# Kernel optimization log

Measured on AMD Instinct MI355X. Metric: run time of the kernel, lower is better.

The kernel has to match this reference:

```python
import jax, jax.numpy as jnp
import numpy as np

B, N, C, H = 8, 1024, 768, 12
D = C // H
SCALE = D ** -0.5


def _norm_unbiased(t):
    # per-head-dim standardization with torch's default unbiased std (ddof=1)
    mu = t.mean(axis=-1, keepdims=True)
    var = ((t - mu) ** 2).sum(axis=-1, keepdims=True) / (t.shape[-1] - 1)
    return (t - mu) / jnp.sqrt(var)


def setup_inputs() -> dict:
    key = jax.random.key(0)
    kx, kq, kp, kb = jax.random.split(key, 4)
    x = jax.random.normal(kx, (B, N, C), dtype=jnp.float32)
    # nn.Linear default init ~ U(-1/sqrt(fan_in), 1/sqrt(fan_in)); scale suffices
    s = 1.0 / np.sqrt(C)
    qkv_w = jax.random.uniform(kq, (3 * C, C), minval=-s, maxval=s, dtype=jnp.float32)
    proj_w = jax.random.uniform(kp, (C, C), minval=-s, maxval=s, dtype=jnp.float32)
    proj_b = jax.random.uniform(kb, (C,), minval=-s, maxval=s, dtype=jnp.float32)
    return {"x": x, "qkv_w": qkv_w, "proj_w": proj_w, "proj_b": proj_b}


def reference(x, qkv_w, proj_w, proj_b):
    Bn, Nn, Cn = x.shape
    qkv = x @ qkv_w.T                                   # [B,N,3C]
    qkv = qkv.reshape(Bn, Nn, 3, H, D).transpose(2, 0, 3, 1, 4)  # [3,B,H,N,D]
    q, k, v = qkv[0], qkv[1], qkv[2]
    q = _norm_unbiased(q)
    k = _norm_unbiased(k)
    attn = jax.nn.softmax(jnp.einsum('bhnd,bhmd->bhnm', q, k) * SCALE, axis=-1)
    out = jnp.einsum('bhnm,bhmd->bhnd', attn, v)        # [B,H,N,D]
    out = out.transpose(0, 2, 1, 3).reshape(Bn, Nn, Cn)  # [B,N,C]
    return out @ proj_w.T + proj_b
```

## Files before the change

kernel.cpp:

```cpp
#include <hip/hip_runtime.h>
#include <hip/hip_bf16.h>
#include <stdint.h>

typedef unsigned short u16;
typedef __attribute__((ext_vector_type(8))) short bf16x8;
typedef __attribute__((ext_vector_type(4))) float f32x4;

#define GLDS16(gsrc, ldst) \
  __builtin_amdgcn_global_load_lds((const __attribute__((address_space(1))) uint32_t*)(gsrc), \
                                   (__attribute__((address_space(3))) uint32_t*)(ldst), 16, 0, 0)

__device__ __forceinline__ u16 f2bf(float f) {
  unsigned u = __float_as_uint(f);
  return (u16)((u + 0x7fffu + ((u >> 16) & 1u)) >> 16);
}
__device__ __forceinline__ u16 f2bfr(float f) {
  return (u16)((__float_as_uint(f) + 0x8000u) >> 16);
}
__device__ __forceinline__ float bf2f(u16 v) {
  return __uint_as_float(((unsigned)v) << 16);
}

__global__ void cvt_f2b4(const float* __restrict__ in, u16* __restrict__ out, int n4) {
  int i = blockIdx.x * 256 + threadIdx.x;
  if (i < n4) {
    float4 v = ((const float4*)in)[i];
    ushort4 r;
    r.x = f2bf(v.x); r.y = f2bf(v.y); r.z = f2bf(v.z); r.w = f2bf(v.w);
    ((ushort4*)out)[i] = r;
  }
}

#define GEMM_PREAMBLE(AP, BP)                                              \
  __shared__ __align__(16) u16 As[3][128 * 32];                            \
  __shared__ __align__(16) u16 Bs[3][128 * 32];                            \
  const int tid  = threadIdx.x;                                            \
  const int lane = tid & 63;                                               \
  const int w    = tid >> 6;                                               \
  const int wr   = w >> 1, wc = w & 1;                                     \
  const int m0 = blockIdx.x * 128;                                         \
  const int n0 = blockIdx.y * 128;                                         \
  f32x4 acc[4][4];                                                         \
  for (int m = 0; m < 4; ++m)                                              \
    for (int n = 0; n < 4; ++n) acc[m][n] = (f32x4){0.f, 0.f, 0.f, 0.f};   \
  const int rsel = lane >> 2;                                              \
  const int koff = (((lane & 3) ^ ((lane >> 3) & 3))) * 8;                 \
  const int fr   = lane & 15;                                              \
  const int hi   = lane >> 4;                                              \
  const int slot = (hi ^ ((fr >> 1) & 3)) * 8;                             \
  auto stage = [&](int buf, int kt) {                                      \
    _Pragma("unroll")                                                      \
    for (int t = 0; t < 2; ++t) {                                          \
      const int seg = w * 2 + t;                                           \
      const int rr  = seg * 16 + rsel;                                     \
      GLDS16(AP + (size_t)(m0 + rr) * 768 + kt * 32 + koff,                \
             (char*)As[buf] + seg * 1024);                                 \
      GLDS16(BP + (size_t)(n0 + rr) * 768 + kt * 32 + koff,                \
             (char*)Bs[buf] + seg * 1024);                                 \
    }                                                                      \
  };                                                                       \
  stage(0, 0); stage(1, 1);                                                \
  asm volatile("s_waitcnt vmcnt(4)" ::: "memory");                         \
  __builtin_amdgcn_s_barrier();                                            \
  for (int kt = 0; kt < 24; ++kt) {                                        \
    const int cb = kt % 3;                                                 \
    if (kt + 2 < 24) stage((kt + 2) % 3, kt + 2);                          \
    bf16x8 af[4], bg[4];                                                   \
    _Pragma("unroll")                                                      \
    for (int m = 0; m < 4; ++m)                                            \
      af[m] = *(const bf16x8*)(As[cb] + (wr * 64 + m * 16 + fr) * 32 + slot);\
    _Pragma("unroll")                                                      \
    for (int n = 0; n < 4; ++n)                                            \
      bg[n] = *(const bf16x8*)(Bs[cb] + (wc * 64 + n * 16 + fr) * 32 + slot);\
    _Pragma("unroll")                                                      \
    for (int m = 0; m < 4; ++m)                                            \
      _Pragma("unroll")                                                    \
      for (int n = 0; n < 4; ++n)                                          \
        acc[m][n] = __builtin_amdgcn_mfma_f32_16x16x32_bf16(af[m], bg[n], acc[m][n], 0, 0, 0); \
    if (kt < 23) {                                                         \
      if (kt < 22) asm volatile("s_waitcnt vmcnt(4)" ::: "memory");        \
      else         asm volatile("s_waitcnt vmcnt(0)" ::: "memory");        \
      __builtin_amdgcn_s_barrier();                                        \
    }                                                                      \
  }

__global__ __launch_bounds__(256, 3)
void gemm_qkv(const u16* __restrict__ A, const u16* __restrict__ Bm,
              u16* __restrict__ qb, u16* __restrict__ kb, u16* __restrict__ vt)
{
  GEMM_PREAMBLE(A, Bm)
  const int b     = m0 >> 10;
  const int nrow0 = (m0 & 1023) + wr * 64 + hi * 4;
  const int sec   = n0 / 768;
  const int csb   = (n0 % 768) + wc * 64;
  const int hh    = csb >> 6;
  if (sec < 2) {
    u16* base = (sec == 0 ? qb : kb) + ((size_t)(b * 12 + hh) << 16);
#pragma unroll
    for (int m = 0; m < 4; ++m)
#pragma unroll
      for (int i = 0; i < 4; ++i) {
        float t0 = acc[m][0][i], t1 = acc[m][1][i], t2 = acc[m][2][i], t3 = acc[m][3][i];
        float sum = (t0 + t1) + (t2 + t3);
        sum += __shfl_xor(sum, 1, 64); sum += __shfl_xor(sum, 2, 64);
        sum += __shfl_xor(sum, 4, 64); sum += __shfl_xor(sum, 8, 64);
        const float mu = sum * (1.f / 64.f);
        t0 -= mu; t1 -= mu; t2 -= mu; t3 -= mu;
        float ss = t0 * t0 + t1 * t1 + t2 * t2 + t3 * t3;
        ss += __shfl_xor(ss, 1, 64); ss += __shfl_xor(ss, 2, 64);
        ss += __shfl_xor(ss, 4, 64); ss += __shfl_xor(ss, 8, 64);
        const float scl = rsqrtf(ss * (1.f / 63.f));
        ushort4 pk;
        pk.x = f2bf(t0 * scl); pk.y = f2bf(t1 * scl);
        pk.z = f2bf(t2 * scl); pk.w = f2bf(t3 * scl);
        *(ushort4*)(base + (size_t)(nrow0 + m * 16 + i) * 64 + fr * 4) = pk;
      }
  } else {
    u16* base = vt + ((size_t)(b * 12 + hh) << 16);
#pragma unroll
    for (int nf = 0; nf < 4; ++nf) {
      const int d = nf * 16 + fr;
#pragma unroll
      for (int m = 0; m < 4; ++m) {
        const int vrow = nrow0 + m * 16;
        ushort4 pk;
        pk.x = f2bf(acc[m][nf][0]); pk.y = f2bf(acc[m][nf][1]);
        pk.z = f2bf(acc[m][nf][2]); pk.w = f2bf(acc[m][nf][3]);
        *(ushort4*)(base + (size_t)d * 1024 + vrow) = pk;
      }
    }
  }
}

__global__ __launch_bounds__(256, 3)
void gemm_proj(const u16* __restrict__ A, const u16* __restrict__ Bm,
               const float* __restrict__ bias, float* __restrict__ Cout)
{
  GEMM_PREAMBLE(A, Bm)
  const int r0 = m0 + wr * 64 + hi * 4;
  const int c0 = n0 + wc * 64 + fr;
#pragma unroll
  for (int nf = 0; nf < 4; ++nf) {
    const float bv = bias[c0 + nf * 16];
#pragma unroll
    for (int m = 0; m < 4; ++m)
#pragma unroll
      for (int i = 0; i < 4; ++i)
        Cout[(size_t)(r0 + m * 16 + i) * 768 + c0 + nf * 16] = acc[m][nf][i] + bv;
  }
}

__global__ __launch_bounds__(256, 4)
void attn_fwd(const u16* __restrict__ q, const u16* __restrict__ k,
              const u16* __restrict__ vt, u16* __restrict__ out)
{
  __shared__ __align__(16) u16 Ks[2][64 * 64];
  __shared__ __align__(16) u16 VTs[2][64 * 64];
  __shared__ __align__(16) u16 Ps[4][16 * 64];
  const int tid = threadIdx.x, lane = tid & 63, w = tid >> 6;
  const int bid = (blockIdx.x & 7) * 192 + (blockIdx.x >> 3);
  const int qt = bid & 15;
  const int bh = bid >> 4;
  const int b = bh / 12, h = bh % 12;
  const int fr = lane & 15;
  const int hi = lane >> 4;
  const int fk = hi * 8;

  bf16x8 aq[2];
  {
    const int qrow = qt * 64 + w * 16 + fr;
    const u16* qp = q + ((size_t)bh * 1024 + qrow) * 64;
#pragma unroll
    for (int kk = 0; kk < 2; ++kk)
      aq[kk] = *(const bf16x8*)(qp + kk * 32 + fk);
  }

  bf16x8 ones;
#pragma unroll
  for (int j = 0; j < 8; ++j) ones[j] = (short)0x3F80;

  f32x4 o[4];
  for (int n = 0; n < 4; ++n) o[n] = (f32x4){0.f, 0.f, 0.f, 0.f};
  f32x4 o5 = (f32x4){0.f, 0.f, 0.f, 0.f};

  const int srow = lane >> 3;
  const int sc   = ((lane & 7) ^ srow) * 8;
  const u16* kg = k  + (size_t)bh * 65536;
  const u16* vg = vt + (size_t)bh * 65536;

  auto stage = [&](int buf, int kt) {
#pragma unroll
    for (int t = 0; t < 2; ++t) {
      const int seg = w * 2 + t;
      const int rr = seg * 8 + srow;
      GLDS16(kg + (size_t)(kt * 64 + rr) * 64 + sc,  (char*)Ks[buf]  + seg * 1024);
      GLDS16(vg + (size_t)rr * 1024 + kt * 64 + sc,  (char*)VTs[buf] + seg * 1024);
    }
  };

  int cur = 0;
  stage(0, 0);
  for (int kt = 0; kt < 16; ++kt) {
    __syncthreads();
    if (kt < 15) stage(cur ^ 1, kt + 1);

    f32x4 s[4];
#pragma unroll
    for (int n = 0; n < 4; ++n) s[n] = (f32x4){0.f, 0.f, 0.f, 0.f};
#pragma unroll
    for (int n = 0; n < 4; ++n)
#pragma unroll
      for (int kk = 0; kk < 2; ++kk) {
        bf16x8 bk = *(const bf16x8*)(Ks[cur] + (n * 16 + fr) * 64 + (((kk * 4 + hi) ^ (fr & 7)) * 8));
        s[n] = __builtin_amdgcn_mfma_f32_16x16x32_bf16(aq[kk], bk, s[n], 0, 0, 0);
      }

#pragma unroll
    for (int n = 0; n < 4; ++n)
#pragma unroll
      for (int i = 0; i < 4; ++i) {
        const float p = __expf(s[n][i] * 0.125f);
        const int row = hi * 4 + i;
        const int swc = (n * 2 + (fr >> 3)) ^ (row & 7);
        Ps[w][row * 64 + swc * 8 + (fr & 7)] = f2bfr(p);
      }

#pragma unroll
    for (int kk = 0; kk < 2; ++kk) {
      bf16x8 ap = *(const bf16x8*)(&Ps[w][fr * 64 + (((kk * 4 + hi) ^ (fr & 7)) * 8)]);
      o5 = __builtin_amdgcn_mfma_f32_16x16x32_bf16(ap, ones, o5, 0, 0, 0);
#pragma unroll
      for (int n = 0; n < 4; ++n) {
        bf16x8 bv = *(const bf16x8*)(VTs[cur] + (n * 16 + fr) * 64 + (((kk * 4 + hi) ^ (fr & 7)) * 8));
        o[n] = __builtin_amdgcn_mfma_f32_16x16x32_bf16(ap, bv, o[n], 0, 0, 0);
      }
    }
    cur ^= 1;
  }

  float inv[4];
#pragma unroll
  for (int i = 0; i < 4; ++i) inv[i] = 1.f / o5[i];
  const int orow0 = qt * 64 + w * 16 + hi * 4;
#pragma unroll
  for (int n = 0; n < 4; ++n)
#pragma unroll
    for (int i = 0; i < 4; ++i)
      out[((size_t)b * 1024 + orow0 + i) * 768 + h * 64 + n * 16 + fr] = f2bfr(o[n][i] * inv[i]);
}

extern "C" void kernel_launch(void* const* d_in, const int* in_sizes, int n_in,
                              void* d_out, int out_size, void* d_ws, size_t ws_size,
                              hipStream_t stream)
{
  (void)in_sizes; (void)n_in; (void)out_size; (void)ws_size;
  const float* x      = (const float*)d_in[0];
  const float* qkv_w  = (const float*)d_in[1];
  const float* proj_w = (const float*)d_in[2];
  const float* proj_b = (const float*)d_in[3];
  float* out = (float*)d_out;

  char* p = (char*)d_ws;
  auto take = [&](size_t bytes) { char* r = p; p += (bytes + 255) & ~(size_t)255; return r; };
  u16* xb   = (u16*)take((size_t)8192 * 768 * 2);
  u16* wqb  = (u16*)take((size_t)2304 * 768 * 2);
  u16* wpb  = (u16*)take((size_t)768 * 768 * 2);
  u16* qb   = (u16*)take((size_t)8192 * 768 * 2);
  u16* kb   = (u16*)take((size_t)8192 * 768 * 2);
  u16* vtb  = (u16*)take((size_t)8192 * 768 * 2);
  u16* aob  = (u16*)take((size_t)8192 * 768 * 2);

  cvt_f2b4<<<6144, 256, 0, stream>>>(x, xb, 8192 * 768 / 4);
  cvt_f2b4<<<1728, 256, 0, stream>>>(qkv_w, wqb, 2304 * 768 / 4);
  cvt_f2b4<<<576,  256, 0, stream>>>(proj_w, wpb, 768 * 768 / 4);

  gemm_qkv<<<dim3(64, 18), 256, 0, stream>>>(xb, wqb, qb, kb, vtb);
  attn_fwd<<<1536, 256, 0, stream>>>(qb, kb, vtb, aob);
  gemm_proj<<<dim3(64, 6), 256, 0, stream>>>(aob, wpb, proj_b, out);
}
```

Measured before the change: 198.4 us.

## Merge fp32-to-bf16 conversions into one launch, drop GEMM LDS swizzle, add setprio

Replaces three conversion kernel launches with a single kernel that dispatches on the global thread index to convert x, qkv_w and proj_w. This saves launch overhead and tail effects. Removes the XOR swizzle from the GEMM LDS staging and fragment reads, which simplifies address math but may add LDS bank conflicts. Wraps the MFMA phases of the attention loop in s_setprio raises to favour matrix issue across waves.

Result: no change. 195.4 us (-1.5%).

```diff
diff --git a/kernel.cpp b/kernel.cpp
--- a/kernel.cpp
+++ b/kernel.cpp
@@ -21,14 +21,19 @@
   return __uint_as_float(((unsigned)v) << 16);
 }
 
-__global__ void cvt_f2b4(const float* __restrict__ in, u16* __restrict__ out, int n4) {
+__global__ void cvt_all(const float* __restrict__ x, const float* __restrict__ wq,
+                        const float* __restrict__ wp, u16* __restrict__ xb,
+                        u16* __restrict__ wqb, u16* __restrict__ wpb) {
   int i = blockIdx.x * 256 + threadIdx.x;
-  if (i < n4) {
-    float4 v = ((const float4*)in)[i];
-    ushort4 r;
-    r.x = f2bf(v.x); r.y = f2bf(v.y); r.z = f2bf(v.z); r.w = f2bf(v.w);
-    ((ushort4*)out)[i] = r;
-  }
+  const float* src; u16* dst; int off;
+  if (i < 1572864)       { src = x;  dst = xb;  off = i; }
+  else if (i < 2015232)  { src = wq; dst = wqb; off = i - 1572864; }
+  else if (i < 2162688)  { src = wp; dst = wpb; off = i - 2015232; }
+  else return;
+  float4 v = ((const float4*)src)[off];
+  ushort4 r;
+  r.x = f2bf(v.x); r.y = f2bf(v.y); r.z = f2bf(v.z); r.w = f2bf(v.w);
+  ((ushort4*)dst)[off] = r;
 }
 
 #define GEMM_PREAMBLE(AP, BP)                                              \
@@ -44,10 +49,10 @@
   for (int m = 0; m < 4; ++m)                                              \
     for (int n = 0; n < 4; ++n) acc[m][n] = (f32x4){0.f, 0.f, 0.f, 0.f};   \
   const int rsel = lane >> 2;                                              \
-  const int koff = (((lane & 3) ^ ((lane >> 3) & 3))) * 8;                 \
+  const int koff = (lane & 3) * 8;                                         \
   const int fr   = lane & 15;                                              \
   const int hi   = lane >> 4;                                              \
-  const int slot = (hi ^ ((fr >> 1) & 3)) * 8;                             \
+  const int fk   = hi * 8;                                                 \
   auto stage = [&](int buf, int kt) {                                      \
     _Pragma("unroll")                                                      \
     for (int t = 0; t < 2; ++t) {                                          \
@@ -68,10 +73,10 @@
     bf16x8 af[4], bg[4];                                                   \
     _Pragma("unroll")                                                      \
     for (int m = 0; m < 4; ++m)                                            \
-      af[m] = *(const bf16x8*)(As[cb] + (wr * 64 + m * 16 + fr) * 32 + slot);\
+      af[m] = *(const bf16x8*)(As[cb] + (wr * 64 + m * 16 + fr) * 32 + fk);\
     _Pragma("unroll")                                                      \
     for (int n = 0; n < 4; ++n)                                            \
-      bg[n] = *(const bf16x8*)(Bs[cb] + (wc * 64 + n * 16 + fr) * 32 + slot);\
+      bg[n] = *(const bf16x8*)(Bs[cb] + (wc * 64 + n * 16 + fr) * 32 + fk);\
     _Pragma("unroll")                                                      \
     for (int m = 0; m < 4; ++m)                                            \
       _Pragma("unroll")                                                    \
@@ -207,6 +212,7 @@
     f32x4 s[4];
 #pragma unroll
     for (int n = 0; n < 4; ++n) s[n] = (f32x4){0.f, 0.f, 0.f, 0.f};
+    __builtin_amdgcn_s_setprio(1);
 #pragma unroll
     for (int n = 0; n < 4; ++n)
 #pragma unroll
@@ -214,6 +220,7 @@
         bf16x8 bk = *(const bf16x8*)(Ks[cur] + (n * 16 + fr) * 64 + (((kk * 4 + hi) ^ (fr & 7)) * 8));
         s[n] = __builtin_amdgcn_mfma_f32_16x16x32_bf16(aq[kk], bk, s[n], 0, 0, 0);
       }
+    __builtin_amdgcn_s_setprio(0);
 
 #pragma unroll
     for (int n = 0; n < 4; ++n)
@@ -225,6 +232,7 @@
         Ps[w][row * 64 + swc * 8 + (fr & 7)] = f2bfr(p);
       }
 
+    __builtin_amdgcn_s_setprio(1);
 #pragma unroll
     for (int kk = 0; kk < 2; ++kk) {
       bf16x8 ap = *(const bf16x8*)(&Ps[w][fr * 64 + (((kk * 4 + hi) ^ (fr & 7)) * 8)]);
@@ -235,6 +243,7 @@
         o[n] = __builtin_amdgcn_mfma_f32_16x16x32_bf16(ap, bv, o[n], 0, 0, 0);
       }
     }
+    __builtin_amdgcn_s_setprio(0);
     cur ^= 1;
   }
 
@@ -270,10 +279,7 @@
   u16* vtb  = (u16*)take((size_t)8192 * 768 * 2);
   u16* aob  = (u16*)take((size_t)8192 * 768 * 2);
 
-  cvt_f2b4<<<6144, 256, 0, stream>>>(x, xb, 8192 * 768 / 4);
-  cvt_f2b4<<<1728, 256, 0, stream>>>(qkv_w, wqb, 2304 * 768 / 4);
-  cvt_f2b4<<<576,  256, 0, stream>>>(proj_w, wpb, 768 * 768 / 4);
-
+  cvt_all<<<8448, 256, 0, stream>>>(x, qkv_w, proj_w, xb, wqb, wpb);
   gemm_qkv<<<dim3(64, 18), 256, 0, stream>>>(xb, wqb, qb, kb, vtb);
   attn_fwd<<<1536, 256, 0, stream>>>(qb, kb, vtb, aob);
   gemm_proj<<<dim3(64, 6), 256, 0, stream>>>(aob, wpb, proj_b, out);
```
